# Optimization experiments

Hardware: AMD Instinct MI355X
Metric: run time of the kernel (lower is better)

## Reference

```python
import jax, jax.numpy as jnp
import numpy as np

JIT = 1e-4
LOG2PI = float(np.log(2.0 * np.pi))
BETA = 1e5
LOC_RADIUS = 5.0


def gaspari_cohn(radius, D):
    i = np.arange(D)
    dist = np.minimum(np.abs(i[:, None] - i[None, :]), D - np.abs(i[:, None] - i[None, :])).astype(np.float64)
    z = dist / radius
    zs = np.maximum(z, 1e-12)
    g1 = 1.0 - 5.0 / 3 * z**2 + 5.0 / 8 * z**3 + 0.5 * z**4 - 0.25 * z**5
    g2 = 4.0 - 5.0 * z + 5.0 / 3 * z**2 + 5.0 / 8 * z**3 - 0.5 * z**4 + 1.0 / 12 * z**5 - 2.0 / (3.0 * zs)
    return np.where(z < 1.0, g1, np.where(z < 2.0, g2, 0.0)).astype(np.float32)


def sq_dist(x, z):
    # x: [..., n, d], z: [..., m, d] (broadcastable)
    x2 = jnp.sum(x * x, -1)[..., :, None]
    z2 = jnp.sum(z * z, -1)[..., None, :]
    d2 = x2 + z2 - 2.0 * jnp.matmul(x, jnp.swapaxes(z, -1, -2))
    return jnp.maximum(d2, 0.0)


def setup_inputs():
    key = jax.random.key(0)
    ks = jax.random.split(key, 12)
    D, dy, M, N, B, T = 32, 32, 128, 128, 8, 48
    ips = jax.random.normal(ks[0], (D, M, D), dtype=jnp.float32)
    H = jnp.eye(dy, D, dtype=jnp.float32)
    lengthscale = jnp.full((D,), 2.0, dtype=jnp.float32)
    outputscale = jnp.ones((D,), dtype=jnp.float32)
    q_mu = 0.1 * jax.random.normal(ks[1], (D, M), dtype=jnp.float32)
    q_L = jnp.tril(0.02 * jax.random.normal(ks[2], (D, M, M), dtype=jnp.float32), -1) + 0.1 * jnp.eye(M, dtype=jnp.float32)[None]
    q_noise = jnp.full((D,), 0.05**2, dtype=jnp.float32)
    r_noise = jnp.full((dy,), 0.1**2, dtype=jnp.float32)
    x0 = jax.random.normal(ks[3], (N, D, B, D), dtype=jnp.float32)
    y = 0.5 * jax.random.normal(ks[4], (B, T, dy), dtype=jnp.float32)
    eps_u = jax.random.normal(ks[5], (N, D, M), dtype=jnp.float32)
    eps_f = jax.random.normal(ks[6], (T, N, D, B), dtype=jnp.float32)
    eps_q = jax.random.normal(ks[7], (T, B, N, D), dtype=jnp.float32)
    eps_r = jax.random.normal(ks[8], (T, B, N, dy), dtype=jnp.float32)
    return {"ips": ips, "H": H, "lengthscale": lengthscale, "outputscale": outputscale,
            "q_mu": q_mu, "q_L": q_L, "q_noise": q_noise, "r_noise": r_noise,
            "x0": x0, "y": y, "eps_u": eps_u, "eps_f": eps_f, "eps_q": eps_q, "eps_r": eps_r}


def _forward(ips, H, lengthscale, outputscale, q_mu, q_L, q_noise, r_noise, x0, y, eps_u, eps_f, eps_q, eps_r):
    N, D, B, _ = x0.shape
    M = ips.shape[1]
    dy = y.shape[-1]
    taper = jnp.asarray(gaspari_cohn(LOC_RADIUS, D))
    ls = lengthscale[:, None, None]
    osc = outputscale[:, None, None]
    zs = ips / ls  # [D, M, D]
    Kzz = osc * jnp.exp(-0.5 * sq_dist(zs, zs)) + JIT * jnp.eye(M, dtype=x0.dtype)  # [D,M,M]
    # U ~ q(u): consistent sampling of inducing outputs per ensemble member
    U = q_mu[None] + jnp.einsum('dmk,ndk->ndm', q_L, eps_u)                 # [N,D,M]
    A = jnp.linalg.solve(Kzz[None], U[..., None])[..., 0]                    # Kzz^{-1} u, [N,D,M]
    # KL(q(u) || N(0, Kzz)) summed over tasks
    Lzz = jnp.linalg.cholesky(Kzz)
    Sq = q_L @ jnp.swapaxes(q_L, -1, -2)
    trace = jnp.sum(jnp.diagonal(jnp.linalg.solve(Kzz, Sq), axis1=-2, axis2=-1))
    mah = jnp.sum(q_mu * jnp.linalg.solve(Kzz, q_mu[..., None])[..., 0])
    logdetK = 2.0 * jnp.sum(jnp.log(jnp.diagonal(Lzz, axis1=-2, axis2=-1)))
    logdetS = 2.0 * jnp.sum(jnp.log(jnp.abs(jnp.diagonal(q_L, axis1=-2, axis2=-1))))
    kl = 0.5 * (trace + mah - D * M + logdetK - logdetS)

    q_sd = jnp.sqrt(q_noise)
    r_sd = jnp.sqrt(r_noise)
    R = jnp.diag(r_noise)
    Ht = H.T
    eyeB = jnp.eye(B, dtype=x0.dtype)

    def step(carry, inp):
        x_prev, ll = carry
        y_t, ef, eq, er = inp
        # ---- GP prediction (conditioned on sampled U) ----
        xq = x_prev / lengthscale[None, :, None, None]                       # [N,D,B,D]
        Kxz = outputscale[None, :, None, None] * jnp.exp(-0.5 * sq_dist(xq, zs[None]))  # [N,D,B,M]
        Kxx = outputscale[None, :, None, None] * jnp.exp(-0.5 * sq_dist(xq, xq))        # [N,D,B,B]
        mean = jnp.einsum('ndbm,ndm->ndb', Kxz, A)
        V = jnp.linalg.solve(Kzz[None], jnp.swapaxes(Kxz, -1, -2))           # [N,D,M,B]
        cov = Kxx - jnp.matmul(Kxz, V) + JIT * eyeB
        Lc = jnp.linalg.cholesky(cov)
        f = mean + jnp.einsum('ndbc,ndc->ndb', Lc, ef)                       # rsample, [N,D,B]
        X = jnp.transpose(f, (2, 0, 1))                                      # [B,N,D]
        X = X + eq * q_sd                                                    # + chol(Q) noise
        Xm = jnp.mean(X, axis=-2, keepdims=True)                             # [B,1,D]
        Xc = X - Xm
        P = taper * (jnp.swapaxes(Xc, -1, -2) @ Xc) / (N - 1)                # localized cov [B,D,D]
        # ---- EnKF update ----
        S = H @ P @ Ht + R                                                   # [B,dy,dy]
        Ls = jnp.linalg.cholesky(S)
        resid = y_t - (Xm @ Ht)[:, 0]                                        # [B,dy]
        alpha = jnp.linalg.solve(S, resid[..., None])[..., 0]
        logdetS_t = 2.0 * jnp.sum(jnp.log(jnp.diagonal(Ls, axis1=-2, axis2=-1)), axis=-1)
        ll_t = -0.5 * jnp.sum(dy * LOG2PI + logdetS_t + jnp.sum(resid * alpha, -1))
        PHt = P @ Ht
        K = jnp.swapaxes(jnp.linalg.solve(S, jnp.swapaxes(PHt, -1, -2)), -1, -2)  # [B,D,dy]
        y_pert = y_t[:, None, :] + er * r_sd
        X_post = X + (y_pert - X @ Ht) @ jnp.swapaxes(K, -1, -2)
        Xm_post = jnp.mean(X_post, axis=-2)                                  # [B,D]
        P_post = P - K @ (H @ P)
        x_next = jnp.broadcast_to(Xm_post[None, None], (N, D, B, D))         # ensemble reset to post. mean
        return (x_next, ll + ll_t), (Xm_post, jnp.diagonal(P_post, axis1=-2, axis2=-1))

    ys = jnp.swapaxes(y, 0, 1)  # [T,B,dy]
    (x_final, ll), (fm, fv) = jax.lax.scan(step, (x0, jnp.asarray(0.0, x0.dtype)), (ys, eps_f, eps_q, eps_r))
    filtered_mean = jnp.swapaxes(fm, 0, 1)  # [B,T,D]
    filtered_var = jnp.swapaxes(fv, 0, 1)   # [B,T,D]
    elbo = ll - kl / BETA
    return elbo, x_final, filtered_mean, filtered_var


def reference(ips, H, lengthscale, outputscale, q_mu, q_L, q_noise, r_noise, x0, y, eps_u, eps_f, eps_q, eps_r):
    return _forward(ips, H, lengthscale, outputscale, q_mu, q_L, q_noise, r_noise, x0, y, eps_u, eps_f, eps_q, eps_r)
```

## Files before the change

### kernel.cpp

```cpp
#include <hip/hip_runtime.h>

#define JITF 1e-4f
#define LOG2PIF 1.8378770664093454f

typedef unsigned long long ull;

#define WZSM   0
#define WZS2   131072
#define WKINV  135168
#define WA     659456
#define WXWT   1183744
#define WXMT   1249280
#define WLLB   1249792
#define WKLD   1249824
#define WCNT   1249984
#define OFM 1048577
#define OFV 1060865

__device__ __forceinline__ float dot4f(const float4 a, const float4 b) {
  return fmaf(a.x, b.x, fmaf(a.y, b.y, fmaf(a.z, b.z, a.w * b.w)));
}
__device__ __forceinline__ float4 f4_fma(const float4 a, const float s, const float4 c) {
  return make_float4(fmaf(a.x,s,c.x), fmaf(a.y,s,c.y), fmaf(a.z,s,c.z), fmaf(a.w,s,c.w));
}
__device__ __forceinline__ float4 f4_axpby(const float a, const float4 x, const float b, const float4 y) {
  return make_float4(fmaf(a,x.x,b*y.x), fmaf(a,x.y,b*y.y), fmaf(a,x.z,b*y.z), fmaf(a,x.w,b*y.w));
}
__device__ __forceinline__ float aloadf(const float* p) {
  return __hip_atomic_load((float*)p, __ATOMIC_RELAXED, __HIP_MEMORY_SCOPE_AGENT);
}
__device__ __forceinline__ void astoref(float* p, float v) {
  __hip_atomic_store(p, v, __ATOMIC_RELAXED, __HIP_MEMORY_SCOPE_AGENT);
}
__device__ __forceinline__ void astoreu(ull* p, ull v) {
  __hip_atomic_store(p, v, __ATOMIC_RELAXED, __HIP_MEMORY_SCOPE_AGENT);
}
__device__ __forceinline__ ull packft(float f, int tag) {
  return (ull)__float_as_uint(f) | ((ull)(unsigned)tag << 32);
}
__device__ __forceinline__ float pollft(const ull* p, int tag) {
  ull u = __hip_atomic_load((ull*)p, __ATOMIC_RELAXED, __HIP_MEMORY_SCOPE_AGENT);
  while ((int)(u >> 32) != tag) {
    __builtin_amdgcn_s_sleep(1);
    u = __hip_atomic_load((ull*)p, __ATOMIC_RELAXED, __HIP_MEMORY_SCOPE_AGENT);
  }
  return __uint_as_float((unsigned)u);
}
__device__ __forceinline__ void pollge(const int* p, int target) {
  while (__hip_atomic_load((int*)p, __ATOMIC_RELAXED, __HIP_MEMORY_SCOPE_AGENT) < target)
    __builtin_amdgcn_s_sleep(1);
}

__global__ __launch_bounds__(1024) void k_sweep(
    const float* __restrict__ ips, const float* __restrict__ ls, const float* __restrict__ osc,
    const float* __restrict__ qL, const float* __restrict__ qmu,
    float* __restrict__ zsMg, float* __restrict__ zs2g,
    float* __restrict__ Kinvg, float* __restrict__ kld, int* cnt)
{
  __shared__ float sm[40200];
  float* cur   = sm;
  float* qLs   = sm + 16896;
  float* zsM   = sm + 33792;
  float* rowP0 = sm + 38400;
  float* rowP1 = sm + 38532;
  float* colP0 = sm + 38664;
  float* colP1 = sm + 38792;
  float* qms   = sm + 38920;
  float* zs2   = sm + 39048;
  float* red   = sm + 39176;
  float4* cur4 = (float4*)cur;
  const float4* zsM4 = (const float4*)zsM;
  float4* rowP04 = (float4*)rowP0;
  float4* rowP14 = (float4*)rowP1;
  const int d = blockIdx.x, tid = threadIdx.x;
  const float invl = 1.0f / ls[d], oscd = osc[d];

  if (blockIdx.x == 0) { for (int l = tid; l < 640; l += 1024) cnt[l] = 0; }

  for (int l = tid; l < 4096; l += 1024) {
    int m = l >> 5, k = l & 31;
    zsM[m*36+k] = ips[(d*128+m)*32+k] * invl;
  }
  for (int l = tid; l < 16384; l += 1024)
    qLs[(l>>7)*132 + (l&127)] = qL[d*16384 + l];
  if (tid < 128) qms[tid] = qmu[d*128+tid];
  __syncthreads();
  if (tid < 128) {
    float s = 0.f;
#pragma unroll
    for (int kq = 0; kq < 8; kq++) { float4 v = zsM4[tid*9+kq]; s += dot4f(v, v); }
    zs2[tid] = s; zs2g[d*128+tid] = s;
  }
  for (int l = tid; l < 4096; l += 1024) zsMg[d*4096+l] = zsM[(l>>5)*36 + (l&31)];
  __syncthreads();

  const int i = tid >> 3, q = tid & 7;
  {
    float4 zr[8];
#pragma unroll
    for (int kq = 0; kq < 8; kq++) zr[kq] = zsM4[i*9+kq];
    float z2i = zs2[i];
    for (int jj = 0; jj < 16; jj++) {
      int j = q*16 + jj;
      float dot = 0.f;
#pragma unroll
      for (int kq = 0; kq < 8; kq++) dot += dot4f(zr[kq], zsM4[j*9+kq]);
      float d2 = fmaxf(z2i + zs2[j] - 2.f*dot, 0.f);
      cur[i*132+j] = oscd * expf(-0.5f*d2) + (i == j ? JITF : 0.f);
    }
  }
  __syncthreads();

  float llog = 0.f;
#pragma unroll 1
  for (int kb = 0; kb < 64; kb++) {
    const int k0 = 2*kb, k1 = k0+1;
    if (tid < 33) rowP04[tid] = cur4[k0*33 + tid];
    else if (tid < 66) rowP14[tid-33] = cur4[k1*33 + (tid-33)];
    else if (tid < 194) colP0[tid-66] = cur[(tid-66)*132 + k0];
    else if (tid < 322) colP1[tid-194] = cur[(tid-194)*132 + k1];
    __syncthreads();
    const float a  = rowP0[k0];
    const float bb = rowP0[k1];
    const float c  = rowP1[k1];
    const float det = fmaf(a, c, -bb*bb);
    const float idet = 1.0f/det;
    if (tid == 0) llog += logf(det);
    const float ci0 = colP0[i], ci1 = colP1[i];
    const float w0 = (ci0*c - ci1*bb)*idet;
    const float w1 = (ci1*a - ci0*bb)*idet;
    const bool isk0 = (i == k0), isk1 = (i == k1);
    const int jqp = k0 >> 2;
    const int c0 = k0 & 3;
    auto body = [&](int jq) {
      float4 r0 = rowP04[jq];
      float4 r1 = rowP14[jq];
      float4 nv;
      if (isk0)      nv = f4_axpby(c*idet, r0, -bb*idet, r1);
      else if (isk1) nv = f4_axpby(-bb*idet, r0, a*idet, r1);
      else {
        nv = cur4[i*33+jq];
        nv = f4_fma(r0, -w0, nv);
        nv = f4_fma(r1, -w1, nv);
      }
      if (jq == jqp) {
        float pv0, pv1;
        if (isk0)      { pv0 = -c*idet;  pv1 =  bb*idet; }
        else if (isk1) { pv0 =  bb*idet; pv1 = -a*idet;  }
        else           { pv0 =  w0;      pv1 =  w1;      }
        if (c0 == 0) { nv.x = pv0; nv.y = pv1; }
        else         { nv.z = pv0; nv.w = pv1; }
      }
      cur4[i*33+jq] = nv;
    };
#pragma unroll
    for (int jj = 0; jj < 4; jj++) body(q*4 + jj);
    if (q == 7) body(32);
    __syncthreads();
  }
  for (int e = tid; e < 16384; e += 1024) { int ii = e>>7, jj = e&127; cur[ii*132+jj] = -cur[ii*132+jj]; }
  __syncthreads();
  for (int l = tid; l < 4096; l += 1024) ((float4*)(Kinvg + d*16384))[l] = cur4[(l>>5)*33 + (l&31)];

  if (tid == 0) kld[d] = 0.5f * llog;
  red[tid] = (tid < 128) ? logf(fabsf(qLs[tid*132+tid])) : 0.f;
  __syncthreads();
  for (int s = 512; s > 0; s >>= 1) { if (tid < s) red[tid] += red[tid+s]; __syncthreads(); }
  if (tid == 0) kld[96+d] = red[0];
  __syncthreads();
  {
    float macc = 0.f;
    for (int e = tid; e < 16384; e += 1024) {
      int ii = e >> 7, jj = e & 127;
      macc = fmaf(cur[ii*132+jj], qms[ii]*qms[jj], macc);
    }
    red[tid] = macc;
    __syncthreads();
    for (int s = 512; s > 0; s >>= 1) { if (tid < s) red[tid] += red[tid+s]; __syncthreads(); }
    if (tid == 0) kld[64+d] = red[0];
    __syncthreads();
  }
  {
    float tacc = 0.f;
    for (int e = tid; e < 16384; e += 1024) {
      int ii = e >> 7, k2 = e & 127;
      if (k2 <= ii) {
        float w = 0.f;
        for (int m = k2; m < 128; m++) w = fmaf(cur[ii*132+m], qLs[m*132+k2], w);
        tacc = fmaf(w, qLs[ii*132+k2], tacc);
      }
    }
    red[tid] = tacc;
    __syncthreads();
    for (int s = 512; s > 0; s >>= 1) { if (tid < s) red[tid] += red[tid+s]; __syncthreads(); }
    if (tid == 0) kld[32+d] = red[0];
  }
}

__global__ __launch_bounds__(256) void k_UA(
    const float* __restrict__ qL, const float* __restrict__ qmu, const float* __restrict__ eu,
    const float* __restrict__ Kinv, float* __restrict__ A)
{
  __shared__ float big[16512];
  __shared__ float Us[4128];
  __shared__ float eus[4128];
  const int d = blockIdx.x >> 2, nc = blockIdx.x & 3, tid = threadIdx.x;
  const int n0 = nc * 32;
  for (int l = tid; l < 16384; l += 256) big[(l>>7)*129 + (l&127)] = qL[d*16384 + l];
  for (int l = tid; l < 4096; l += 256)
    eus[(l>>7)*129 + (l&127)] = eu[((n0 + (l>>7))*32 + d)*128 + (l&127)];
  __syncthreads();
  for (int e = tid; e < 4096; e += 256) {
    int nl = e >> 7, m = e & 127;
    float s0 = qmu[d*128 + m], s1 = 0.f, s2 = 0.f, s3 = 0.f;
    int kmax = m + 1, k4 = kmax & ~3, k = 0;
    for (; k < k4; k += 4) {
      s0 = fmaf(big[m*129+k],   eus[nl*129+k],   s0);
      s1 = fmaf(big[m*129+k+1], eus[nl*129+k+1], s1);
      s2 = fmaf(big[m*129+k+2], eus[nl*129+k+2], s2);
      s3 = fmaf(big[m*129+k+3], eus[nl*129+k+3], s3);
    }
    for (; k < kmax; k++) s0 = fmaf(big[m*129+k], eus[nl*129+k], s0);
    Us[nl*129+m] = (s0+s1)+(s2+s3);
  }
  __syncthreads();
  for (int l = tid; l < 16384; l += 256) big[(l>>7)*129 + (l&127)] = Kinv[d*16384 + l];
  __syncthreads();
  for (int e = tid; e < 4096; e += 256) {
    int nl = e >> 7, m = e & 127;
    float s0 = 0.f, s1 = 0.f, s2 = 0.f, s3 = 0.f;
    for (int k = 0; k < 128; k += 4) {
      s0 = fmaf(big[m*129+k],   Us[nl*129+k],   s0);
      s1 = fmaf(big[m*129+k+1], Us[nl*129+k+1], s1);
      s2 = fmaf(big[m*129+k+2], Us[nl*129+k+2], s2);
      s3 = fmaf(big[m*129+k+3], Us[nl*129+k+3], s3);
    }
    A[((n0+nl)*32 + d)*128 + m] = (s0+s1)+(s2+s3);
  }
}

__global__ __launch_bounds__(128) void k_t0gp(
    const float* __restrict__ x0, const float* __restrict__ ls, const float* __restrict__ osc,
    const float* __restrict__ qn, const float* __restrict__ zsMg, const float* __restrict__ zs2g,
    const float* __restrict__ Kinv, const float* __restrict__ A,
    const float* __restrict__ ef, const float* __restrict__ eq, ull* __restrict__ XwT)
{
  __shared__ float xqs[8*36];
  __shared__ float xq2s[8];
  __shared__ float Kxzs[8*132];
  __shared__ float T1s[8*132];
  __shared__ float covs[8][9];
  __shared__ float Lc[8][9];
  __shared__ float Arow[132];
  const float4* xqs4  = (const float4*)xqs;
  const float4* Kxzs4 = (const float4*)Kxzs;
  const float4* T1s4  = (const float4*)T1s;
  const float4* Arow4 = (const float4*)Arow;
  const int n = blockIdx.x >> 5, d = blockIdx.x & 31, tid = threadIdx.x;
  const float invl = 1.0f / ls[d], oscd = osc[d];

  float4 zr[8];
  {
    const float4* zrow = (const float4*)(zsMg + d*4096 + tid*32);
#pragma unroll
    for (int kq = 0; kq < 8; kq++) zr[kq] = zrow[kq];
  }
  const float z2m = zs2g[d*128 + tid];
  for (int l = tid; l < 256; l += 128) {
    int b = l >> 5, k = l & 31;
    xqs[b*36+k] = x0[((n*32+d)*8 + b)*32 + k] * invl;
  }
  Arow[tid] = A[(n*32+d)*128 + tid];
  __syncthreads();
  if (tid < 8) {
    float s = 0.f;
#pragma unroll
    for (int kq = 0; kq < 8; kq++) { float4 v = xqs4[tid*9+kq]; s += dot4f(v, v); }
    xq2s[tid] = s;
  }
  __syncthreads();
  {
#pragma unroll
    for (int b = 0; b < 8; b++) {
      float dot = 0.f;
#pragma unroll
      for (int kq = 0; kq < 8; kq++) dot += dot4f(zr[kq], xqs4[b*9+kq]);
      Kxzs[b*132+tid] = oscd * expf(-0.5f * fmaxf(xq2s[b] + z2m - 2.f*dot, 0.f));
    }
  }
  __syncthreads();
  {
    float a[8] = {0.f,0.f,0.f,0.f,0.f,0.f,0.f,0.f};
    const float* kp = Kinv + d*16384 + tid;
    for (int mq = 0; mq < 32; mq++) {
      float kv0 = kp[(4*mq+0)*128];
      float kv1 = kp[(4*mq+1)*128];
      float kv2 = kp[(4*mq+2)*128];
      float kv3 = kp[(4*mq+3)*128];
#pragma unroll
      for (int b = 0; b < 8; b++) {
        float4 kx = Kxzs4[b*33+mq];
        a[b] = fmaf(kx.x, kv0, fmaf(kx.y, kv1, fmaf(kx.z, kv2, fmaf(kx.w, kv3, a[b]))));
      }
    }
#pragma unroll
    for (int b = 0; b < 8; b++) T1s[b*132+tid] = a[b];
  }
  __syncthreads();
  if (tid < 64) {
    int b = tid >> 3, c = tid & 7;
    float sc = 0.f, dt = 0.f;
#pragma unroll
    for (int mq = 0; mq < 32; mq++) sc += dot4f(T1s4[b*33+mq], Kxzs4[c*33+mq]);
#pragma unroll
    for (int kq = 0; kq < 8; kq++) dt += dot4f(xqs4[b*9+kq], xqs4[c*9+kq]);
    float kxx = oscd * expf(-0.5f * fmaxf(xq2s[b] + xq2s[c] - 2.f*dt, 0.f));
    covs[b][c] = kxx - sc + (b == c ? JITF : 0.f);
  }
  __syncthreads();
  if (tid == 0) {
    for (int a = 0; a < 8; a++) {
      float s = covs[a][a];
      for (int k = 0; k < a; k++) s -= Lc[a][k]*Lc[a][k];
      float la = sqrtf(s);
      Lc[a][a] = la;
      for (int i2 = a+1; i2 < 8; i2++) {
        float s2 = covs[i2][a];
        for (int k = 0; k < a; k++) s2 -= Lc[i2][k]*Lc[a][k];
        Lc[i2][a] = s2 / la;
      }
    }
  }
  __syncthreads();
  if (tid < 8) {
    int b = tid;
    float mv = 0.f;
#pragma unroll
    for (int mq = 0; mq < 32; mq++) mv += dot4f(Kxzs4[b*33+mq], Arow4[mq]);
    float f = mv;
#pragma unroll
    for (int c = 0; c < 8; c++) if (c <= b) f = fmaf(Lc[b][c], ef[(n*32+d)*8 + c], f);
    float X = f + eq[(b*128+n)*32 + d] * sqrtf(qn[d]);
    astoreu(XwT + (d*8+b)*128 + n, packft(X, 0));
  }
}

__global__ __launch_bounds__(1024) void k_scan(
    const float* __restrict__ ls, const float* __restrict__ osc,
    const float* __restrict__ qn, const float* __restrict__ rn,
    const float* __restrict__ y,
    const float* __restrict__ ef, const float* __restrict__ eq, const float* __restrict__ er,
    const float* __restrict__ zsMg, const float* __restrict__ zs2g,
    const float* __restrict__ Kinvg, const float* __restrict__ Ag,
    ull* XwT, ull* xmT, float* llb, const float* __restrict__ kld,
    float* out, int* cnt)
{
  __shared__ float sm[36704];
  const int blk = blockIdx.x, tid = threadIdx.x;

  if (blk < 32) {
    const int d = blk;
    float* KinvS = sm;
    float* AT    = sm + 16512;
    float* KxzS  = sm + 33024;
    float* T1S   = sm + 34080;
    float* xqS   = sm + 35136;
    float* efS   = sm + 35424;
    float* covS  = sm + 36576;
    const float invl = 1.0f/ls[d], oscd = osc[d], qsd = sqrtf(qn[d]);
    const float4* KxzS4 = (const float4*)KxzS;
    const float4* T1S4  = (const float4*)T1S;
    const float4* xqS4  = (const float4*)xqS;

    for (int l = tid; l < 16384; l += 1024)
      KinvS[(l>>7)*129 + (l&127)] = Kinvg[d*16384 + l];
    for (int l = tid; l < 16384; l += 1024) {
      int n = l >> 7, m = l & 127;
      AT[m*129 + n] = Ag[(n*32 + d)*128 + m];
    }

    const int bb = tid >> 7, mn = tid & 127;
    float4 zr[8];
    {
      const float4* zrow = (const float4*)(zsMg + d*4096 + mn*32);
#pragma unroll
      for (int kq = 0; kq < 8; kq++) zr[kq] = zrow[kq];
    }
    const float z2m = zs2g[d*128 + mn];
    __syncthreads();

    for (int t = 1; t < 48; t++) {
      const float v_ef = ef[((t*128 + (tid>>3))*32 + d)*8 + (tid&7)];
      const float v_eq = eq[((t*8+bb)*128 + mn)*32 + d];

      if (tid < 256) {
        float v = pollft(xmT + tid, t-1);
        xqS[(tid>>5)*36 + (tid&31)] = v * invl;
      }
      efS[(tid>>3)*9 + (tid&7)] = v_ef;
      __syncthreads();
      {
        float dot = 0.f, sq = 0.f;
#pragma unroll
        for (int kq = 0; kq < 8; kq++) {
          float4 x4 = xqS4[bb*9+kq];
          dot += dot4f(zr[kq], x4);
          sq  += dot4f(x4, x4);
        }
        KxzS[bb*132+mn] = oscd * expf(-0.5f * fmaxf(sq + z2m - 2.f*dot, 0.f));
      }
      __syncthreads();
      float mv;
      {
        float t1a = 0.f, t1b = 0.f, ma = 0.f, mb2 = 0.f;
#pragma unroll 8
        for (int mm = 0; mm < 128; mm += 2) {
          float kx0 = KxzS[bb*132+mm], kx1 = KxzS[bb*132+mm+1];
          t1a = fmaf(kx0, KinvS[mm*129+mn],     t1a);
          t1b = fmaf(kx1, KinvS[(mm+1)*129+mn], t1b);
          ma  = fmaf(kx0, AT[mm*129+mn],        ma);
          mb2 = fmaf(kx1, AT[(mm+1)*129+mn],    mb2);
        }
        T1S[bb*132+mn] = t1a + t1b;
        mv = ma + mb2;
      }
      __syncthreads();
      if (tid < 64) {
        int b = tid >> 3, c = tid & 7;
        float sc = 0.f, dt = 0.f, sqb = 0.f, sqc = 0.f;
#pragma unroll
        for (int mq = 0; mq < 32; mq++) sc += dot4f(T1S4[b*33+mq], KxzS4[c*33+mq]);
#pragma unroll
        for (int kq = 0; kq < 8; kq++) {
          float4 xb = xqS4[b*9+kq], xc = xqS4[c*9+kq];
          dt += dot4f(xb, xc); sqb += dot4f(xb, xb); sqc += dot4f(xc, xc);
        }
        float kxx = oscd*expf(-0.5f*fmaxf(sqb + sqc - 2.f*dt, 0.f));
        covS[b*9+c] = kxx - sc + (b==c ? JITF : 0.f);
      }
      __syncthreads();
      {
        float Lc[8][8];
        float f = mv;
#pragma unroll
        for (int a = 0; a < 8; a++) {
          float s = covS[a*9+a];
#pragma unroll
          for (int k = 0; k < 8; k++) if (k < a) s -= Lc[a][k]*Lc[a][k];
          float la = sqrtf(s);
          Lc[a][a] = la;
          if (a == bb) f = fmaf(la, efS[mn*9+a], f);
          float ila = 1.0f / la;
#pragma unroll
          for (int i2 = 0; i2 < 8; i2++) if (i2 > a) {
            float s2 = covS[i2*9+a];
#pragma unroll
            for (int k = 0; k < 8; k++) if (k < a) s2 -= Lc[i2][k]*Lc[a][k];
            float lv = s2 * ila;
            Lc[i2][a] = lv;
            if (i2 == bb) f = fmaf(lv, efS[mn*9+a], f);
          }
        }
        f = fmaf(v_eq, qsd, f);
        astoreu(XwT + (d*8+bb)*128 + mn, packft(f, t));
      }
      __syncthreads();
    }
  } else {
    const int b = blk - 32;
    float* XN     = sm;
    float* Ps     = sm + 4224;
    float* Sinvs  = sm + 5376;
    float* taperS = sm + 6432;
    float* mersS  = sm + 7456;
    float* rowP   = sm + 8992;
    float* colP   = sm + 9280;
    float* detS   = sm + 9568;
    float* XmsS   = sm + 9576;
    float* residS = sm + 9608;
    float* miS    = sm + 9640;
    float* rsdS   = sm + 9672;
    float* rnS    = sm + 9704;
    const float4* er4 = (const float4*)er;

    if (tid < 1024) {
      int ii = tid >> 5, jj = tid & 31;
      int ad = ii - jj; if (ad < 0) ad = -ad;
      int dist = (ad < 32 - ad) ? ad : (32 - ad);
      double z = (double)dist / 5.0;
      double z2 = z*z, z3 = z2*z, z4 = z3*z, z5 = z4*z;
      double gval;
      if (z < 1.0) gval = 1.0 - (5.0/3.0)*z2 + (5.0/8.0)*z3 + 0.5*z4 - 0.25*z5;
      else if (z < 2.0) gval = 4.0 - 5.0*z + (5.0/3.0)*z2 + (5.0/8.0)*z3 - 0.5*z4 + (1.0/12.0)*z5 - 2.0/(3.0*z);
      else gval = 0.0;
      taperS[tid] = (float)gval;
    }
    if (tid < 32) { rnS[tid] = rn[tid]; rsdS[tid] = sqrtf(rn[tid]); }
    if (tid < 384) {
      int tt = tid >> 3, jq = tid & 7;
      float sx = 0.f, sy = 0.f, sz = 0.f, sw = 0.f;
      for (int n = 0; n < 128; n++) {
        float4 e = er4[((tt*8+b)*128+n)*8 + jq];
        sx += e.x; sy += e.y; sz += e.z; sw += e.w;
      }
      int o = tt*32 + jq*4;
      mersS[o]   = sx*(1.f/128.f);
      mersS[o+1] = sy*(1.f/128.f);
      mersS[o+2] = sz*(1.f/128.f);
      mersS[o+3] = sw*(1.f/128.f);
    }
    __syncthreads();

    float llacc = 0.f;
    const int i = tid >> 5, j = tid & 31;
    for (int t = 0; t < 48; t++) {
      float yv = 0.f;
      if (tid < 32) yv = y[(b*48+t)*32 + tid];
      {
        const ull* base = XwT + (i*8+b)*128;
        float x0v = pollft(base + 2*j,      t);
        float x1v = pollft(base + 2*j + 1,  t);
        float x2v = pollft(base + 2*j + 64, t);
        float x3v = pollft(base + 2*j + 65, t);
        float s4 = (x0v+x1v)+(x2v+x3v);
#pragma unroll
        for (int mk = 1; mk <= 16; mk <<= 1) s4 += __shfl_xor(s4, mk, 64);
        float mu = s4 * (1.f/128.f);
        if (j == 0) XmsS[i] = mu;
        XN[(2*j)*33+i]    = x0v - mu;
        XN[(2*j+1)*33+i]  = x1v - mu;
        XN[(2*j+64)*33+i] = x2v - mu;
        XN[(2*j+65)*33+i] = x3v - mu;
      }
      __syncthreads();
      float val;
      {
        float a0 = 0.f, a1 = 0.f;
#pragma unroll 4
        for (int n = 0; n < 128; n += 2) {
          a0 = fmaf(XN[n*33+i],     XN[n*33+j],     a0);
          a1 = fmaf(XN[(n+1)*33+i], XN[(n+1)*33+j], a1);
        }
        float pv = taperS[i*32+j] * (a0+a1) * (1.f/127.f);
        Ps[i*36+j] = pv;
        val = pv + ((i==j) ? rnS[i] : 0.f);
      }
#pragma unroll 1
      for (int kb = 0; kb < 8; kb++) {
        const int k0 = kb*4;
        float* rowPb = rowP + (kb&1)*144;
        float* colPb = colP + (kb&1)*144;
        if (i >= k0 && i < k0+4) rowPb[(i-k0)*36 + j] = val;
        if (j >= k0 && j < k0+4) colPb[(j-k0)*36 + i] = val;
        __syncthreads();
        float p00 = rowPb[0*36+k0+0], p01 = rowPb[0*36+k0+1], p02 = rowPb[0*36+k0+2], p03 = rowPb[0*36+k0+3];
        float p11 = rowPb[1*36+k0+1], p12 = rowPb[1*36+k0+2], p13 = rowPb[1*36+k0+3];
        float p22 = rowPb[2*36+k0+2], p23 = rowPb[2*36+k0+3], p33 = rowPb[3*36+k0+3];
        float deta = fmaf(p00, p11, -p01*p01);
        float ia = 1.0f/deta;
        float ai00 = p11*ia, ai01 = -p01*ia, ai11 = p00*ia;
        float m00 = ai00*p02 + ai01*p12;
        float m01 = ai00*p03 + ai01*p13;
        float m10 = ai01*p02 + ai11*p12;
        float m11 = ai01*p03 + ai11*p13;
        float s00 = p22 - (p02*m00 + p12*m10);
        float s01 = p23 - (p02*m01 + p12*m11);
        float s11 = p33 - (p03*m01 + p13*m11);
        float dets = fmaf(s00, s11, -s01*s01);
        float is = 1.0f/dets;
        float si00 = s11*is, si01 = -s01*is, si11 = s00*is;
        float n00 = m00*si00 + m01*si01;
        float n01 = m00*si01 + m01*si11;
        float n10 = m10*si00 + m11*si01;
        float n11 = m10*si01 + m11*si11;
        float q00 = ai00 + n00*m00 + n01*m01;
        float q01 = ai01 + n00*m10 + n01*m11;
        float q11 = ai11 + n10*m10 + n11*m11;
        const float PI[4][4] = {
          {  q00,  q01, -n00, -n01 },
          {  q01,  q11, -n10, -n11 },
          { -n00, -n10, si00, si01 },
          { -n01, -n11, si01, si11 }
        };
        if (tid == 0) detS[kb] = deta * dets;
        float cI[4], rJ[4];
#pragma unroll
        for (int a = 0; a < 4; a++) { cI[a] = colPb[a*36 + i]; rJ[a] = rowPb[a*36 + j]; }
        float w[4];
#pragma unroll
        for (int bq = 0; bq < 4; bq++)
          w[bq] = cI[0]*PI[0][bq] + cI[1]*PI[1][bq] + cI[2]*PI[2][bq] + cI[3]*PI[3][bq];
        float interior = val - (w[0]*rJ[0] + w[1]*rJ[1] + w[2]*rJ[2] + w[3]*rJ[3]);
        const int r = i - k0, c = j - k0;
        const bool ip = (r >= 0 && r < 4), jp = (c >= 0 && c < 4);
        float pr[4], pc[4];
#pragma unroll
        for (int bq = 0; bq < 4; bq++) {
          pr[bq] = (r==0) ? PI[0][bq] : (r==1) ? PI[1][bq] : (r==2) ? PI[2][bq] : PI[3][bq];
          pc[bq] = (c==0) ? PI[bq][0] : (c==1) ? PI[bq][1] : (c==2) ? PI[bq][2] : PI[bq][3];
        }
        float rowv = pr[0]*rJ[0] + pr[1]*rJ[1] + pr[2]*rJ[2] + pr[3]*rJ[3];
        float colv = cI[0]*pc[0] + cI[1]*pc[1] + cI[2]*pc[2] + cI[3]*pc[3];
        float prc  = (c==0) ? pr[0] : (c==1) ? pr[1] : (c==2) ? pr[2] : pr[3];
        float nv = interior;
        if (ip) nv = rowv;
        if (jp) nv = colv;
        if (ip && jp) nv = -prc;
        val = nv;
      }
      Sinvs[i*33+j] = -val;
      if (tid < 32) {
        float rs = yv - XmsS[tid];
        residS[tid] = rs;
        miS[tid] = fmaf(mersS[t*32+tid], rsdS[tid], rs);
      }
      __syncthreads();
      if (tid < 32) {
        float bt = 0.f;
#pragma unroll
        for (int k = 0; k < 32; k++) bt = fmaf(Sinvs[tid*33+k], miS[k], bt);
        float xmp = XmsS[tid] + miS[tid] - rnS[tid]*bt;
        out[OFM + (b*48+t)*32 + tid] = xmp;
        out[OFV + (b*48+t)*32 + tid] = rnS[tid] - rnS[tid]*rnS[tid]*Sinvs[tid*33+tid];
        astoreu(xmT + b*32 + tid, packft(xmp, t));
      } else if (tid < 64) {
        int ii = tid - 32;
        float al = 0.f;
#pragma unroll
        for (int k = 0; k < 32; k++) al = fmaf(Sinvs[ii*33+k], residS[k], al);
        float contrib = al * residS[ii] + ((ii < 8) ? logf(detS[ii]) : 0.f);
#pragma unroll
        for (int mk = 1; mk <= 16; mk <<= 1) contrib += __shfl_xor(contrib, mk, 64);
        if (ii == 0) {
          llacc += -0.5f*(32.f*LOG2PIF + contrib);
          if (t == 47) astoref(llb + b, llacc);
        }
      }
      __syncthreads();
    }
    if (tid == 0)
      __hip_atomic_store(cnt + (32+b)*16, 1, __ATOMIC_RELEASE, __HIP_MEMORY_SCOPE_AGENT);
  }

  if (tid < 256) sm[tid] = pollft(xmT + tid, 47);
  __syncthreads();
  for (int v = blk*1024 + tid; v < 1048576; v += 40960)
    out[1 + v] = sm[v & 255];
  if (blk == 32 && tid == 0) {
    for (int b2 = 0; b2 < 8; b2++) pollge(cnt + (32+b2)*16, 1);
    double ll = 0.0;
    for (int i2 = 0; i2 < 8; i2++) ll += (double)aloadf(llb + i2);
    double ldK = 0.0, tr = 0.0, mah = 0.0, ldS = 0.0;
    for (int d2 = 0; d2 < 32; d2++) {
      ldK += (double)kld[d2];
      tr  += (double)kld[32+d2];
      mah += (double)kld[64+d2];
      ldS += (double)kld[96+d2];
    }
    double klv = 0.5*(tr + mah - 4096.0 + 2.0*ldK - 2.0*ldS);
    out[0] = (float)(ll - klv/100000.0);
  }
}

extern "C" void kernel_launch(void* const* d_in, const int* in_sizes, int n_in,
                              void* d_out, int out_size, void* d_ws, size_t ws_size,
                              hipStream_t stream) {
  const float* ips = (const float*)d_in[0];
  const float* ls  = (const float*)d_in[2];
  const float* osc = (const float*)d_in[3];
  const float* qmu = (const float*)d_in[4];
  const float* qL  = (const float*)d_in[5];
  const float* qn  = (const float*)d_in[6];
  const float* rn  = (const float*)d_in[7];
  const float* x0  = (const float*)d_in[8];
  const float* y   = (const float*)d_in[9];
  const float* eu  = (const float*)d_in[10];
  const float* ef  = (const float*)d_in[11];
  const float* eq  = (const float*)d_in[12];
  const float* er  = (const float*)d_in[13];
  float* out = (float*)d_out;
  float* ws  = (float*)d_ws;

  float* w_zsm  = ws + WZSM;
  float* w_zs2  = ws + WZS2;
  float* w_kinv = ws + WKINV;
  float* w_A    = ws + WA;
  ull*   w_xwt  = (ull*)(ws + WXWT);
  ull*   w_xmt  = (ull*)(ws + WXMT);
  float* w_llb  = ws + WLLB;
  float* w_kld  = ws + WKLD;
  int*   w_cnt  = (int*)(ws + WCNT);

  k_sweep<<<32, 1024, 0, stream>>>(ips, ls, osc, qL, qmu, w_zsm, w_zs2, w_kinv, w_kld, w_cnt);
  k_UA<<<128, 256, 0, stream>>>(qL, qmu, eu, w_kinv, w_A);
  k_t0gp<<<4096, 128, 0, stream>>>(x0, ls, osc, qn, w_zsm, w_zs2, w_kinv, w_A, ef, eq, w_xwt);
  void* args[] = { (void*)&ls, (void*)&osc, (void*)&qn, (void*)&rn, (void*)&y,
                   (void*)&ef, (void*)&eq, (void*)&er, (void*)&w_zsm, (void*)&w_zs2,
                   (void*)&w_kinv, (void*)&w_A, (void*)&w_xwt, (void*)&w_xmt, (void*)&w_llb,
                   (void*)&w_kld, (void*)&out, (void*)&w_cnt };
  hipLaunchCooperativeKernel((void*)k_scan, dim3(40), dim3(1024), args, 0, stream);
}
```

Before: 1.885 ms.

## Fuse UA into sweep kernel and replace tagged polling with counter flags

The separate U/A kernel is merged into the tail of k_sweep, which reuses the q_L and K^-1 tiles already held in shared memory and drops one launch. In the cooperative scan kernel, per-element tagged 64-bit values polled individually are replaced by plain float buffers guarded by per-block release counters, so consumers wait on a few flags and then read packed float2 data. The GP-block inner loop is also reworked to read float4 of Kxz with four accumulators. Risks are memory-ordering correctness with relaxed loads after the counter waits, and extra serial work in the 32 sweep blocks.

```diff
diff --git a/kernel.cpp b/kernel.cpp
--- a/kernel.cpp
+++ b/kernel.cpp
@@ -9,11 +9,11 @@
 #define WZS2   131072
 #define WKINV  135168
 #define WA     659456
-#define WXWT   1183744
-#define WXMT   1249280
-#define WLLB   1249792
-#define WKLD   1249824
-#define WCNT   1249984
+#define WXW    1183744
+#define WXM    1216512
+#define WLLB   1216768
+#define WKLD   1216800
+#define WCNT   1216960
 #define OFM 1048577
 #define OFV 1060865
 
@@ -32,42 +32,35 @@
 __device__ __forceinline__ void astoref(float* p, float v) {
   __hip_atomic_store(p, v, __ATOMIC_RELAXED, __HIP_MEMORY_SCOPE_AGENT);
 }
-__device__ __forceinline__ void astoreu(ull* p, ull v) {
-  __hip_atomic_store(p, v, __ATOMIC_RELAXED, __HIP_MEMORY_SCOPE_AGENT);
-}
-__device__ __forceinline__ ull packft(float f, int tag) {
-  return (ull)__float_as_uint(f) | ((ull)(unsigned)tag << 32);
-}
-__device__ __forceinline__ float pollft(const ull* p, int tag) {
-  ull u = __hip_atomic_load((ull*)p, __ATOMIC_RELAXED, __HIP_MEMORY_SCOPE_AGENT);
-  while ((int)(u >> 32) != tag) {
-    __builtin_amdgcn_s_sleep(1);
-    u = __hip_atomic_load((ull*)p, __ATOMIC_RELAXED, __HIP_MEMORY_SCOPE_AGENT);
-  }
-  return __uint_as_float((unsigned)u);
+__device__ __forceinline__ ull aloadu(const ull* p) {
+  return __hip_atomic_load((ull*)p, __ATOMIC_RELAXED, __HIP_MEMORY_SCOPE_AGENT);
 }
 __device__ __forceinline__ void pollge(const int* p, int target) {
   while (__hip_atomic_load((int*)p, __ATOMIC_RELAXED, __HIP_MEMORY_SCOPE_AGENT) < target)
     __builtin_amdgcn_s_sleep(1);
 }
+__device__ __forceinline__ void gsignal(int* p, int val, int tid) {
+  __syncthreads();
+  if (tid == 0) __hip_atomic_store(p, val, __ATOMIC_RELEASE, __HIP_MEMORY_SCOPE_AGENT);
+}
 
 __global__ __launch_bounds__(1024) void k_sweep(
     const float* __restrict__ ips, const float* __restrict__ ls, const float* __restrict__ osc,
-    const float* __restrict__ qL, const float* __restrict__ qmu,
+    const float* __restrict__ qL, const float* __restrict__ qmu, const float* __restrict__ eu,
     float* __restrict__ zsMg, float* __restrict__ zs2g,
-    float* __restrict__ Kinvg, float* __restrict__ kld, int* cnt)
+    float* __restrict__ Kinvg, float* __restrict__ Ag, float* __restrict__ kld, int* cnt)
 {
-  __shared__ float sm[40200];
+  __shared__ float sm[39816];
   float* cur   = sm;
   float* qLs   = sm + 16896;
-  float* zsM   = sm + 33792;
-  float* rowP0 = sm + 38400;
-  float* rowP1 = sm + 38532;
-  float* colP0 = sm + 38664;
-  float* colP1 = sm + 38792;
-  float* qms   = sm + 38920;
-  float* zs2   = sm + 39048;
-  float* red   = sm + 39176;
+  float* zsM   = sm + 33408;
+  float* rowP0 = sm + 38016;
+  float* rowP1 = sm + 38148;
+  float* colP0 = sm + 38280;
+  float* colP1 = sm + 38408;
+  float* qms   = sm + 38536;
+  float* zs2   = sm + 38664;
+  float* red   = sm + 38792;
   float4* cur4 = (float4*)cur;
   const float4* zsM4 = (const float4*)zsM;
   float4* rowP04 = (float4*)rowP0;
@@ -82,7 +75,7 @@
     zsM[m*36+k] = ips[(d*128+m)*32+k] * invl;
   }
   for (int l = tid; l < 16384; l += 1024)
-    qLs[(l>>7)*132 + (l&127)] = qL[d*16384 + l];
+    qLs[(l>>7)*129 + (l&127)] = qL[d*16384 + l];
   if (tid < 128) qms[tid] = qmu[d*128+tid];
   __syncthreads();
   if (tid < 128) {
@@ -163,7 +156,7 @@
   for (int l = tid; l < 4096; l += 1024) ((float4*)(Kinvg + d*16384))[l] = cur4[(l>>5)*33 + (l&31)];
 
   if (tid == 0) kld[d] = 0.5f * llog;
-  red[tid] = (tid < 128) ? logf(fabsf(qLs[tid*132+tid])) : 0.f;
+  red[tid] = (tid < 128) ? logf(fabsf(qLs[tid*129+tid])) : 0.f;
   __syncthreads();
   for (int s = 512; s > 0; s >>= 1) { if (tid < s) red[tid] += red[tid+s]; __syncthreads(); }
   if (tid == 0) kld[96+d] = red[0];
@@ -186,8 +179,8 @@
       int ii = e >> 7, k2 = e & 127;
       if (k2 <= ii) {
         float w = 0.f;
-        for (int m = k2; m < 128; m++) w = fmaf(cur[ii*132+m], qLs[m*132+k2], w);
-        tacc = fmaf(w, qLs[ii*132+k2], tacc);
+        for (int m = k2; m < 128; m++) w = fmaf(cur[ii*132+m], qLs[m*129+k2], w);
+        tacc = fmaf(w, qLs[ii*129+k2], tacc);
       }
     }
     red[tid] = tacc;
@@ -195,47 +188,42 @@
     for (int s = 512; s > 0; s >>= 1) { if (tid < s) red[tid] += red[tid+s]; __syncthreads(); }
     if (tid == 0) kld[32+d] = red[0];
   }
-}
-
-__global__ __launch_bounds__(256) void k_UA(
-    const float* __restrict__ qL, const float* __restrict__ qmu, const float* __restrict__ eu,
-    const float* __restrict__ Kinv, float* __restrict__ A)
-{
-  __shared__ float big[16512];
-  __shared__ float Us[4128];
-  __shared__ float eus[4128];
-  const int d = blockIdx.x >> 2, nc = blockIdx.x & 3, tid = threadIdx.x;
-  const int n0 = nc * 32;
-  for (int l = tid; l < 16384; l += 256) big[(l>>7)*129 + (l&127)] = qL[d*16384 + l];
-  for (int l = tid; l < 4096; l += 256)
-    eus[(l>>7)*129 + (l&127)] = eu[((n0 + (l>>7))*32 + d)*128 + (l&127)];
-  __syncthreads();
-  for (int e = tid; e < 4096; e += 256) {
-    int nl = e >> 7, m = e & 127;
-    float s0 = qmu[d*128 + m], s1 = 0.f, s2 = 0.f, s3 = 0.f;
-    int kmax = m + 1, k4 = kmax & ~3, k = 0;
-    for (; k < k4; k += 4) {
-      s0 = fmaf(big[m*129+k],   eus[nl*129+k],   s0);
-      s1 = fmaf(big[m*129+k+1], eus[nl*129+k+1], s1);
-      s2 = fmaf(big[m*129+k+2], eus[nl*129+k+2], s2);
-      s3 = fmaf(big[m*129+k+3], eus[nl*129+k+3], s3);
-    }
-    for (; k < kmax; k++) s0 = fmaf(big[m*129+k], eus[nl*129+k], s0);
-    Us[nl*129+m] = (s0+s1)+(s2+s3);
-  }
-  __syncthreads();
-  for (int l = tid; l < 16384; l += 256) big[(l>>7)*129 + (l&127)] = Kinv[d*16384 + l];
-  __syncthreads();
-  for (int e = tid; e < 4096; e += 256) {
-    int nl = e >> 7, m = e & 127;
-    float s0 = 0.f, s1 = 0.f, s2 = 0.f, s3 = 0.f;
-    for (int k = 0; k < 128; k += 4) {
-      s0 = fmaf(big[m*129+k],   Us[nl*129+k],   s0);
-      s1 = fmaf(big[m*129+k+1], Us[nl*129+k+1], s1);
-      s2 = fmaf(big[m*129+k+2], Us[nl*129+k+2], s2);
-      s3 = fmaf(big[m*129+k+3], Us[nl*129+k+3], s3);
-    }
-    A[((n0+nl)*32 + d)*128 + m] = (s0+s1)+(s2+s3);
+  {
+    float* eus = zsM;
+    float* Uc  = zsM + 2112;
+    __syncthreads();
+    for (int c = 0; c < 8; c++) {
+      const int n0 = c*16;
+      for (int l = tid; l < 2048; l += 1024)
+        eus[(l>>7)*132 + (l&127)] = eu[((n0 + (l>>7))*32 + d)*128 + (l&127)];
+      __syncthreads();
+      for (int e = tid; e < 2048; e += 1024) {
+        int nl = e >> 7, m = e & 127;
+        float s0 = qms[m], s1 = 0.f, s2 = 0.f, s3 = 0.f;
+        int kmax = m+1, k4 = kmax & ~3, k = 0;
+        for (; k < k4; k += 4) {
+          s0 = fmaf(qLs[m*129+k],   eus[nl*132+k],   s0);
+          s1 = fmaf(qLs[m*129+k+1], eus[nl*132+k+1], s1);
+          s2 = fmaf(qLs[m*129+k+2], eus[nl*132+k+2], s2);
+          s3 = fmaf(qLs[m*129+k+3], eus[nl*132+k+3], s3);
+        }
+        for (; k < kmax; k++) s0 = fmaf(qLs[m*129+k], eus[nl*132+k], s0);
+        Uc[nl*132+m] = (s0+s1)+(s2+s3);
+      }
+      __syncthreads();
+      for (int e = tid; e < 2048; e += 1024) {
+        int nl = e >> 7, m = e & 127;
+        float s0 = 0.f, s1 = 0.f, s2 = 0.f, s3 = 0.f;
+        for (int k = 0; k < 128; k += 4) {
+          s0 = fmaf(cur[k*132+m],     Uc[nl*132+k],   s0);
+          s1 = fmaf(cur[(k+1)*132+m], Uc[nl*132+k+1], s1);
+          s2 = fmaf(cur[(k+2)*132+m], Uc[nl*132+k+2], s2);
+          s3 = fmaf(cur[(k+3)*132+m], Uc[nl*132+k+3], s3);
+        }
+        Ag[((n0+nl)*32 + d)*128 + m] = (s0+s1)+(s2+s3);
+      }
+      __syncthreads();
+    }
   }
 }
 
@@ -243,7 +231,7 @@
     const float* __restrict__ x0, const float* __restrict__ ls, const float* __restrict__ osc,
     const float* __restrict__ qn, const float* __restrict__ zsMg, const float* __restrict__ zs2g,
     const float* __restrict__ Kinv, const float* __restrict__ A,
-    const float* __restrict__ ef, const float* __restrict__ eq, ull* __restrict__ XwT)
+    const float* __restrict__ ef, const float* __restrict__ eq, float* __restrict__ Xw)
 {
   __shared__ float xqs[8*36];
   __shared__ float xq2s[8];
@@ -341,7 +329,7 @@
 #pragma unroll
     for (int c = 0; c < 8; c++) if (c <= b) f = fmaf(Lc[b][c], ef[(n*32+d)*8 + c], f);
     float X = f + eq[(b*128+n)*32 + d] * sqrtf(qn[d]);
-    astoreu(XwT + (d*8+b)*128 + n, packft(X, 0));
+    Xw[(d*8+b)*128 + n] = X;
   }
 }
 
@@ -352,7 +340,7 @@
     const float* __restrict__ ef, const float* __restrict__ eq, const float* __restrict__ er,
     const float* __restrict__ zsMg, const float* __restrict__ zs2g,
     const float* __restrict__ Kinvg, const float* __restrict__ Ag,
-    ull* XwT, ull* xmT, float* llb, const float* __restrict__ kld,
+    float* Xw, float* xm, float* llb, const float* __restrict__ kld,
     float* out, int* cnt)
 {
   __shared__ float sm[36704];
@@ -371,6 +359,7 @@
     const float4* KxzS4 = (const float4*)KxzS;
     const float4* T1S4  = (const float4*)T1S;
     const float4* xqS4  = (const float4*)xqS;
+    const ull* xm_u = (const ull*)xm;
 
     for (int l = tid; l < 16384; l += 1024)
       KinvS[(l>>7)*129 + (l&127)] = Kinvg[d*16384 + l];
@@ -393,9 +382,14 @@
       const float v_ef = ef[((t*128 + (tid>>3))*32 + d)*8 + (tid&7)];
       const float v_eq = eq[((t*8+bb)*128 + mn)*32 + d];
 
-      if (tid < 256) {
-        float v = pollft(xmT + tid, t-1);
-        xqS[(tid>>5)*36 + (tid&31)] = v * invl;
+      if (tid < 8) pollge(cnt + (32+tid)*16, t);
+      __syncthreads();
+      if (tid < 128) {
+        ull u = aloadu(xm_u + tid);
+        float2 f = __builtin_bit_cast(float2, u);
+        int b2 = tid >> 4, k2 = (tid & 15)*2;
+        xqS[b2*36 + k2]     = f.x * invl;
+        xqS[b2*36 + k2 + 1] = f.y * invl;
       }
       efS[(tid>>3)*9 + (tid&7)] = v_ef;
       __syncthreads();
@@ -412,17 +406,23 @@
       __syncthreads();
       float mv;
       {
-        float t1a = 0.f, t1b = 0.f, ma = 0.f, mb2 = 0.f;
+        float t1[4] = {0.f,0.f,0.f,0.f};
+        float me[4] = {0.f,0.f,0.f,0.f};
 #pragma unroll 8
-        for (int mm = 0; mm < 128; mm += 2) {
-          float kx0 = KxzS[bb*132+mm], kx1 = KxzS[bb*132+mm+1];
-          t1a = fmaf(kx0, KinvS[mm*129+mn],     t1a);
-          t1b = fmaf(kx1, KinvS[(mm+1)*129+mn], t1b);
-          ma  = fmaf(kx0, AT[mm*129+mn],        ma);
-          mb2 = fmaf(kx1, AT[(mm+1)*129+mn],    mb2);
-        }
-        T1S[bb*132+mn] = t1a + t1b;
-        mv = ma + mb2;
+        for (int mq = 0; mq < 32; mq++) {
+          float4 kx = KxzS4[bb*33+mq];
+          int mm = mq*4;
+          t1[0] = fmaf(kx.x, KinvS[mm*129+mn],     t1[0]);
+          t1[1] = fmaf(kx.y, KinvS[(mm+1)*129+mn], t1[1]);
+          t1[2] = fmaf(kx.z, KinvS[(mm+2)*129+mn], t1[2]);
+          t1[3] = fmaf(kx.w, KinvS[(mm+3)*129+mn], t1[3]);
+          me[0] = fmaf(kx.x, AT[mm*129+mn],        me[0]);
+          me[1] = fmaf(kx.y, AT[(mm+1)*129+mn],    me[1]);
+          me[2] = fmaf(kx.z, AT[(mm+2)*129+mn],    me[2]);
+          me[3] = fmaf(kx.w, AT[(mm+3)*129+mn],    me[3]);
+        }
+        T1S[bb*132+mn] = (t1[0]+t1[1])+(t1[2]+t1[3]);
+        mv = (me[0]+me[1])+(me[2]+me[3]);
       }
       __syncthreads();
       if (tid < 64) {
@@ -462,10 +462,12 @@
           }
         }
         f = fmaf(v_eq, qsd, f);
-        astoreu(XwT + (d*8+bb)*128 + mn, packft(f, t));
-      }
-      __syncthreads();
-    }
+        astoref(Xw + (d*8+bb)*128 + mn, f);
+      }
+      gsignal(cnt + d*16, t, tid);
+    }
+    if (tid < 8) pollge(cnt + (32+tid)*16, 48);
+    __syncthreads();
   } else {
     const int b = blk - 32;
     float* XN     = sm;
@@ -482,6 +484,7 @@
     float* rsdS   = sm + 9672;
     float* rnS    = sm + 9704;
     const float4* er4 = (const float4*)er;
+    const ull* Xw_u = (const ull*)Xw;
 
     if (tid < 1024) {
       int ii = tid >> 5, jj = tid & 31;
@@ -516,21 +519,22 @@
     for (int t = 0; t < 48; t++) {
       float yv = 0.f;
       if (tid < 32) yv = y[(b*48+t)*32 + tid];
+      if (t > 0) { if (tid < 32) pollge(cnt + tid*16, t); }
+      __syncthreads();
       {
-        const ull* base = XwT + (i*8+b)*128;
-        float x0v = pollft(base + 2*j,      t);
-        float x1v = pollft(base + 2*j + 1,  t);
-        float x2v = pollft(base + 2*j + 64, t);
-        float x3v = pollft(base + 2*j + 65, t);
-        float s4 = (x0v+x1v)+(x2v+x3v);
+        ull u0 = aloadu(Xw_u + (i*8+b)*64 + j);
+        ull u1 = aloadu(Xw_u + (i*8+b)*64 + j + 32);
+        float2 f0 = __builtin_bit_cast(float2, u0);
+        float2 f1 = __builtin_bit_cast(float2, u1);
+        float s4 = (f0.x+f0.y)+(f1.x+f1.y);
 #pragma unroll
         for (int mk = 1; mk <= 16; mk <<= 1) s4 += __shfl_xor(s4, mk, 64);
         float mu = s4 * (1.f/128.f);
         if (j == 0) XmsS[i] = mu;
-        XN[(2*j)*33+i]    = x0v - mu;
-        XN[(2*j+1)*33+i]  = x1v - mu;
-        XN[(2*j+64)*33+i] = x2v - mu;
-        XN[(2*j+65)*33+i] = x3v - mu;
+        XN[(2*j)*33+i]    = f0.x - mu;
+        XN[(2*j+1)*33+i]  = f0.y - mu;
+        XN[(2*j+64)*33+i] = f1.x - mu;
+        XN[(2*j+65)*33+i] = f1.y - mu;
       }
       __syncthreads();
       float val;
@@ -622,7 +626,7 @@
         float xmp = XmsS[tid] + miS[tid] - rnS[tid]*bt;
         out[OFM + (b*48+t)*32 + tid] = xmp;
         out[OFV + (b*48+t)*32 + tid] = rnS[tid] - rnS[tid]*rnS[tid]*Sinvs[tid*33+tid];
-        astoreu(xmT + b*32 + tid, packft(xmp, t));
+        astoref(xm + b*32 + tid, xmp);
       } else if (tid < 64) {
         int ii = tid - 32;
         float al = 0.f;
@@ -636,18 +640,21 @@
           if (t == 47) astoref(llb + b, llacc);
         }
       }
-      __syncthreads();
-    }
-    if (tid == 0)
-      __hip_atomic_store(cnt + (32+b)*16, 1, __ATOMIC_RELEASE, __HIP_MEMORY_SCOPE_AGENT);
-  }
-
-  if (tid < 256) sm[tid] = pollft(xmT + tid, 47);
+      gsignal(cnt + (32+b)*16, t+1, tid);
+    }
+    if (tid < 8) pollge(cnt + (32+tid)*16, 48);
+    __syncthreads();
+  }
+
+  if (tid < 128) {
+    ull u = aloadu((const ull*)xm + tid);
+    float2 f = __builtin_bit_cast(float2, u);
+    sm[2*tid] = f.x; sm[2*tid+1] = f.y;
+  }
   __syncthreads();
   for (int v = blk*1024 + tid; v < 1048576; v += 40960)
     out[1 + v] = sm[v & 255];
   if (blk == 32 && tid == 0) {
-    for (int b2 = 0; b2 < 8; b2++) pollge(cnt + (32+b2)*16, 1);
     double ll = 0.0;
     for (int i2 = 0; i2 < 8; i2++) ll += (double)aloadf(llb + i2);
     double ldK = 0.0, tr = 0.0, mah = 0.0, ldS = 0.0;
@@ -685,18 +692,17 @@
   float* w_zs2  = ws + WZS2;
   float* w_kinv = ws + WKINV;
   float* w_A    = ws + WA;
-  ull*   w_xwt  = (ull*)(ws + WXWT);
-  ull*   w_xmt  = (ull*)(ws + WXMT);
+  float* w_Xw   = ws + WXW;
+  float* w_xm   = ws + WXM;
   float* w_llb  = ws + WLLB;
   float* w_kld  = ws + WKLD;
   int*   w_cnt  = (int*)(ws + WCNT);
 
-  k_sweep<<<32, 1024, 0, stream>>>(ips, ls, osc, qL, qmu, w_zsm, w_zs2, w_kinv, w_kld, w_cnt);
-  k_UA<<<128, 256, 0, stream>>>(qL, qmu, eu, w_kinv, w_A);
-  k_t0gp<<<4096, 128, 0, stream>>>(x0, ls, osc, qn, w_zsm, w_zs2, w_kinv, w_A, ef, eq, w_xwt);
+  k_sweep<<<32, 1024, 0, stream>>>(ips, ls, osc, qL, qmu, eu, w_zsm, w_zs2, w_kinv, w_A, w_kld, w_cnt);
+  k_t0gp<<<4096, 128, 0, stream>>>(x0, ls, osc, qn, w_zsm, w_zs2, w_kinv, w_A, ef, eq, w_Xw);
   void* args[] = { (void*)&ls, (void*)&osc, (void*)&qn, (void*)&rn, (void*)&y,
                    (void*)&ef, (void*)&eq, (void*)&er, (void*)&w_zsm, (void*)&w_zs2,
-                   (void*)&w_kinv, (void*)&w_A, (void*)&w_xwt, (void*)&w_xmt, (void*)&w_llb,
+                   (void*)&w_kinv, (void*)&w_A, (void*)&w_Xw, (void*)&w_xm, (void*)&w_llb,
                    (void*)&w_kld, (void*)&out, (void*)&w_cnt };
   hipLaunchCooperativeKernel((void*)k_scan, dim3(40), dim3(1024), args, 0, stream);
 }
```

After: 2.100 ms. 11.4% more time.
